# Kernel tuning notes

Measured on AMD Instinct MI355X. Metric: run time of the kernel, lower is better.

The kernel has to match this reference:

```python
import jax, jax.numpy as jnp
import numpy as np

B, N, D, H = 2048, 512, 128, 256
TRADE_K, N_BEST, CONF_TH = 10, 50, 0.05


def setup_inputs() -> dict:
    key = jax.random.key(0)
    ks = jax.random.split(key, 5)
    return {
        "signal_features": jax.random.normal(ks[0], (B, N, D), jnp.float32),
        "spread": jax.random.uniform(ks[1], (B, N), jnp.float32, minval=1e-4, maxval=0.01),
        "volatility": jax.random.uniform(ks[2], (B, N), jnp.float32, minval=1e-4, maxval=0.05),
        "W1": jax.random.normal(ks[3], (D, H), jnp.float32) / np.sqrt(D).astype(np.float32),
        "b1": jnp.zeros((H,), jnp.float32),
        "W2": jax.random.normal(ks[4], (H, 1), jnp.float32) / np.sqrt(H).astype(np.float32),
        "b2": jnp.zeros((1,), jnp.float32),
    }


def _scatter_mask(idx, n):
    # idx: [B, k] int32 -> bool mask [B, n] with True at idx positions
    b = idx.shape[0]
    return jnp.zeros((b, n), bool).at[jnp.arange(b)[:, None], idx].set(True)


def reference(signal_features, spread, volatility, W1, b1, W2, b2):
    # signal predictor: per-asset MLP with sigmoid head -> [B, N]
    h = jax.nn.relu(jnp.einsum('bnd,dh->bnh', signal_features, W1) + b1)
    signal_repr = jax.nn.sigmoid(jnp.einsum('bnh,ho->bno', h, W2)[..., 0] + b2[0])
    ls_score = signal_repr - 0.5  # allow_short_positions=True

    n_best = min(N_BEST, N)
    valid_spread = jnp.isfinite(spread) & (spread > 0)
    ratio = jnp.where(valid_spread, volatility / (spread + 1e-8), -jnp.inf)
    _, best_idx = jax.lax.top_k(ratio, n_best)
    universe_mask = _scatter_mask(best_idx, N)
    # rows with no valid spread: whole universe allowed
    universe_mask = universe_mask | ~valid_spread.any(axis=1, keepdims=True)

    masked_abs = jnp.where(universe_mask, jnp.abs(ls_score), -jnp.inf)
    k = min(TRADE_K, n_best)
    _, top_idx = jax.lax.top_k(masked_abs, k)
    mask = _scatter_mask(top_idx, N)

    selected = jnp.where(mask, ls_score, 0.0)
    action = selected / (jnp.sum(jnp.abs(selected), axis=1, keepdims=True) + 1e-8)

    confidence = masked_abs.max(axis=1)
    confidence = jnp.where(jnp.isfinite(confidence), confidence, 0.0)
    take_trade = (confidence >= CONF_TH).astype(action.dtype)[:, None]
    action = action * take_trade
    return action, confidence
```

## Files before the change

kernel.cpp:

```cpp
#include <hip/hip_runtime.h>
#include <hip/hip_bf16.h>
#include <math.h>

#define B_ 2048
#define N_ 512
#define D_ 128
#define H_ 256
#define BANDf 2e-4f

typedef __attribute__((ext_vector_type(8))) short bf16x8;
typedef __attribute__((ext_vector_type(4))) float f32x4;

__device__ __forceinline__ short f2bf(float x) {
    unsigned u = __float_as_uint(x);
    u = u + 0x7fffu + ((u >> 16) & 1u);
    return (short)(u >> 16);
}
__device__ __forceinline__ float bf2f(short h) {
    return __uint_as_float(((unsigned)(unsigned short)h) << 16);
}
__device__ __forceinline__ unsigned cvt_pk_bf16(float a, float b) {
    unsigned r;
    asm("v_cvt_pk_bf16_f32 %0, %1, %2" : "=v"(r) : "v"(a), "v"(b));
    return r;
}
template<int K>
__device__ __forceinline__ float dpp_shr_add(float zz) {
    int s = __builtin_amdgcn_update_dpp(0, __float_as_int(zz), 0x110 | K, 0xf, 0xf, true);
    return zz + __int_as_float(s);
}

__global__ __launch_bounds__(256) void pack_w(const float* __restrict__ W1,
                                              short* __restrict__ WpH,
                                              short* __restrict__ WpL)
{
    int tid = blockIdx.x * 256 + threadIdx.x;
    int l  = tid & 63;
    int ks = (tid >> 6) & 3;
    int nf = tid >> 8;
    int n  = nf * 16 + (l & 15);
    int kb = ks * 32 + ((l >> 4) << 3);
    bf16x8 hi, lo;
    #pragma unroll
    for (int j = 0; j < 8; ++j) {
        float w = W1[(size_t)(kb + j) * H_ + n];
        short h = f2bf(w);
        hi[j] = h;
        lo[j] = f2bf(w - bf2f(h));
    }
    *(bf16x8*)&WpH[(size_t)tid * 8] = hi;
    *(bf16x8*)&WpL[(size_t)tid * 8] = lo;
}

__global__ __launch_bounds__(256, 2) void mlp_mfma(
    const float* __restrict__ X, const short* __restrict__ WpH,
    const short* __restrict__ WpL, const float* __restrict__ b1,
    const float* __restrict__ W2, const float* __restrict__ b2,
    float* __restrict__ ls)
{
    __shared__ short Xh[64 * 128];
    __shared__ short Xl[64 * 128];
    __shared__ float zl[256];

    const int t    = threadIdx.x;
    const int lane = t & 63;
    const int wn   = t >> 6;
    const size_t m0 = (size_t)blockIdx.x * 64;

    const bf16x8* WH = (const bf16x8*)WpH;
    const bf16x8* WL = (const bf16x8*)WpL;

    bf16x8 Bhi[4][4];
    #pragma unroll
    for (int q = 0; q < 4; ++q)
        #pragma unroll
        for (int ks = 0; ks < 4; ++ks)
            Bhi[q][ks] = WH[((wn * 4 + q) * 4 + ks) * 64 + lane];

    bf16x8 Blo[2][4];
    #pragma unroll
    for (int q = 0; q < 4; ++q)
        Blo[0][q] = WL[((wn * 4 + q) * 4 + 0) * 64 + lane];

    {
        const float4* Xg = (const float4*)(X + m0 * D_);
        #pragma unroll
        for (int i = 0; i < 8; ++i) {
            int f = t + i * 256;
            float4 v = Xg[f];
            int row = f >> 5, k0 = (f & 31) << 2;
            unsigned h01 = cvt_pk_bf16(v.x, v.y);
            unsigned h23 = cvt_pk_bf16(v.z, v.w);
            float l0 = v.x - __uint_as_float(h01 << 16);
            float l1 = v.y - __uint_as_float(h01 & 0xffff0000u);
            float l2 = v.z - __uint_as_float(h23 << 16);
            float l3 = v.w - __uint_as_float(h23 & 0xffff0000u);
            unsigned lo01 = cvt_pk_bf16(l0, l1);
            unsigned lo23 = cvt_pk_bf16(l2, l3);
            int sidx = (row * 128 + k0) ^ ((row & 7) << 3);
            *(uint2*)&Xh[sidx] = make_uint2(h01, h23);
            *(uint2*)&Xl[sidx] = make_uint2(lo01, lo23);
        }
    }
    __syncthreads();

    f32x4 acc[4][4];
    #pragma unroll
    for (int mf = 0; mf < 4; ++mf)
        #pragma unroll
        for (int q = 0; q < 4; ++q)
            acc[mf][q] = (f32x4){0.f, 0.f, 0.f, 0.f};

    __builtin_amdgcn_s_setprio(1);
    #pragma unroll
    for (int ks = 0; ks < 4; ++ks) {
        const int cur = ks & 1, nxt = cur ^ 1;
        if (ks < 3) {
            #pragma unroll
            for (int q = 0; q < 4; ++q)
                Blo[nxt][q] = WL[((wn * 4 + q) * 4 + ks + 1) * 64 + lane];
        }
        #pragma unroll
        for (int mf = 0; mf < 4; ++mf) {
            int r = mf * 16 + (lane & 15);
            int sidx = (r * 128 + ks * 32 + ((lane >> 4) << 3)) ^ ((r & 7) << 3);
            bf16x8 Ah = *(const bf16x8*)&Xh[sidx];
            bf16x8 Al = *(const bf16x8*)&Xl[sidx];
            #pragma unroll
            for (int q = 0; q < 4; ++q) {
                acc[mf][q] = __builtin_amdgcn_mfma_f32_16x16x32_bf16(Ah, Bhi[q][ks],  acc[mf][q], 0, 0, 0);
                acc[mf][q] = __builtin_amdgcn_mfma_f32_16x16x32_bf16(Al, Bhi[q][ks],  acc[mf][q], 0, 0, 0);
                acc[mf][q] = __builtin_amdgcn_mfma_f32_16x16x32_bf16(Ah, Blo[cur][q], acc[mf][q], 0, 0, 0);
            }
        }
    }
    __builtin_amdgcn_s_setprio(0);

    float b1v[4], w2v[4];
    #pragma unroll
    for (int q = 0; q < 4; ++q) {
        int c = wn * 64 + q * 16 + (lane & 15);
        b1v[q] = b1[c];
        w2v[q] = W2[c];
    }
    #pragma unroll
    for (int mf = 0; mf < 4; ++mf) {
        #pragma unroll
        for (int i = 0; i < 4; ++i) {
            float zz = 0.f;
            #pragma unroll
            for (int q = 0; q < 4; ++q) {
                float h = acc[mf][q][i] + b1v[q];
                h = h > 0.f ? h : 0.f;
                zz += h * w2v[q];
            }
            zz = dpp_shr_add<1>(zz);
            zz = dpp_shr_add<2>(zz);
            zz = dpp_shr_add<4>(zz);
            zz = dpp_shr_add<8>(zz);
            if ((lane & 15) == 15) zl[wn * 64 + mf * 16 + ((lane >> 4) << 2) + i] = zz;
        }
    }
    __syncthreads();
    if (t < 64) {
        float z = zl[t] + zl[64 + t] + zl[128 + t] + zl[192 + t] + b2[0];
        ls[m0 + t] = 1.f / (1.f + expf(-z)) - 0.5f;
    }
}

__device__ __forceinline__ unsigned f2key(float f) {
    unsigned u = __float_as_uint(f);
    return (u & 0x80000000u) ? ~u : (u | 0x80000000u);
}
__device__ __forceinline__ float key2f(unsigned k) {
    return __uint_as_float((k & 0x80000000u) ? (k & 0x7fffffffu) : ~k);
}
__device__ __forceinline__ int lane_lt_count(unsigned long long m) {
    return __builtin_amdgcn_mbcnt_hi((unsigned)(m >> 32),
           __builtin_amdgcn_mbcnt_lo((unsigned)m, 0));
}

__device__ __forceinline__ void radix_topk(const unsigned (&key)[8], int k,
                                           unsigned &T, int &need)
{
    unsigned prefix = 0, maskhi = 0;
    int kk = k;
    for (int bit = 31; bit >= 0; --bit) {
        unsigned b = 1u << bit;
        int cnt1 = 0;
        #pragma unroll
        for (int j = 0; j < 8; ++j) {
            bool one = ((key[j] & maskhi) == prefix) && (key[j] & b);
            cnt1 += __popcll(__ballot(one));
        }
        if (cnt1 >= kk) prefix |= b; else kk -= cnt1;
        maskhi |= b;
    }
    T = prefix; need = kk;
}

__device__ __forceinline__ void tie_member(const unsigned (&key)[8], unsigned T,
                                           int need, bool (&mem)[8])
{
    int base = 0;
    #pragma unroll
    for (int j = 0; j < 8; ++j) {
        unsigned long long eb = __ballot(key[j] == T);
        int r = base + lane_lt_count(eb);
        mem[j] = (key[j] > T) || ((key[j] == T) && (r < need));
        base += __popcll(eb);
    }
}

__global__ __launch_bounds__(256) void select_kernel(
    const float* __restrict__ ls, const float* __restrict__ spread,
    const float* __restrict__ vol, const float* __restrict__ X,
    const float* __restrict__ W1, const float* __restrict__ b1,
    const float* __restrict__ W2, const float* __restrict__ b2,
    float* __restrict__ action, float* __restrict__ conf_out)
{
    const int t = threadIdx.x;
    const int l = t & 63;
    const int w = t >> 6;
    const int b = blockIdx.x * 4 + w;
    const size_t base = (size_t)b * N_;

    float rv[8], lsv[8];
    unsigned kr[8];
    bool anyv = false;
    #pragma unroll
    for (int j = 0; j < 8; ++j) {
        int n = l + (j << 6);
        float sp = spread[base + n];
        float vo = vol[base + n];
        bool valid = isfinite(sp) && (sp > 0.f);
        rv[j]  = valid ? (vo / (sp + 1e-8f)) : -INFINITY;
        lsv[j] = ls[base + n];
        anyv |= valid;
        kr[j] = f2key(rv[j]);
    }
    bool allow_all = (__any((int)anyv) == 0);

    unsigned T50; int need50;
    radix_topk(kr, 50, T50, need50);
    bool mem50[8];
    tie_member(kr, T50, need50, mem50);

    float mabs[8];
    unsigned km[8];
    #pragma unroll
    for (int j = 0; j < 8; ++j) {
        bool u = allow_all || mem50[j];
        mabs[j] = u ? fabsf(lsv[j]) : -INFINITY;
        km[j] = f2key(mabs[j]);
    }
    unsigned T10; int need10;
    radix_topk(km, 10, T10, need10);
    bool mem10[8];
    tie_member(km, T10, need10, mem10);
    float b10 = key2f(T10);

    float zp = 0.f, cf = -INFINITY;
    #pragma unroll
    for (int j = 0; j < 8; ++j) {
        if (mem10[j]) zp += mabs[j];
        cf = fmaxf(cf, mabs[j]);
    }
    #pragma unroll
    for (int s = 1; s < 64; s <<= 1) {
        zp += __shfl_xor(zp, s, 64);
        cf = fmaxf(cf, __shfl_xor(cf, s, 64));
    }
    float conf = cf;

    bool confclose = fabsf(conf - 0.05f) <= BANDf;
    bool inband[8];
    int nb = 0;
    #pragma unroll
    for (int j = 0; j < 8; ++j) {
        inband[j] = (mabs[j] != -INFINITY) && (fabsf(mabs[j] - b10) <= BANDf);
        nb += __popcll(__ballot(inband[j]));
    }
    bool redo = (nb >= 2) || confclose;

    if (!redo) {
        float cfin  = isfinite(conf) ? conf : 0.f;
        float scale = (cfin >= 0.05f) ? (1.f / (zp + 1e-8f)) : 0.f;
        #pragma unroll
        for (int j = 0; j < 8; ++j) {
            int n = l + (j << 6);
            action[base + n] = mem10[j] ? lsv[j] * scale : 0.f;
        }
        if (l == 0) conf_out[b] = cfin;
        return;
    }

    const float2* xr2 = (const float2*)&X[base * D_];
    float4 bb = *(const float4*)&b1[l * 4];
    float4 ww = *(const float4*)&W2[l * 4];
    const float b2v = b2[0];

    #pragma unroll
    for (int j = 0; j < 8; ++j) {
        bool cand = (nb >= 2 && inband[j]) || (confclose && mabs[j] == conf);
        unsigned long long bal = __ballot(cand);
        while (bal) {
            int s = __ffsll((long long)bal) - 1;
            bal &= bal - 1;
            int asset = s + (j << 6);
            float2 x2 = xr2[(size_t)asset * 64 + l];
            float h0 = 0.f, h1 = 0.f, h2 = 0.f, h3 = 0.f;
            #pragma unroll 16
            for (int kk = 0; kk < D_; ++kk) {
                float xk = __shfl((kk & 1) ? x2.y : x2.x, kk >> 1, 64);
                float4 wv = *(const float4*)&W1[(size_t)kk * H_ + l * 4];
                h0 += xk * wv.x; h1 += xk * wv.y; h2 += xk * wv.z; h3 += xk * wv.w;
            }
            h0 += bb.x; h1 += bb.y; h2 += bb.z; h3 += bb.w;
            float zz = (h0 > 0.f ? h0 : 0.f) * ww.x + (h1 > 0.f ? h1 : 0.f) * ww.y
                     + (h2 > 0.f ? h2 : 0.f) * ww.z + (h3 > 0.f ? h3 : 0.f) * ww.w;
            #pragma unroll
            for (int sh = 1; sh < 64; sh <<= 1) zz += __shfl_xor(zz, sh, 64);
            float val = 1.f / (1.f + expf(-(zz + b2v))) - 0.5f;
            if (l == s) {
                lsv[j]  = val;
                mabs[j] = fabsf(val);
                km[j]   = f2key(mabs[j]);
            }
        }
    }

    unsigned T10b; int need10b;
    radix_topk(km, 10, T10b, need10b);
    bool mem10b[8];
    tie_member(km, T10b, need10b, mem10b);

    float zx = 0.f, cfx = -INFINITY;
    #pragma unroll
    for (int j = 0; j < 8; ++j) {
        if (mem10b[j]) zx += mabs[j];
        cfx = fmaxf(cfx, mabs[j]);
    }
    #pragma unroll
    for (int s = 1; s < 64; s <<= 1) {
        zx += __shfl_xor(zx, s, 64);
        cfx = fmaxf(cfx, __shfl_xor(cfx, s, 64));
    }
    cfx = isfinite(cfx) ? cfx : 0.f;
    float scale = (cfx >= 0.05f) ? (1.f / (zx + 1e-8f)) : 0.f;
    #pragma unroll
    for (int j = 0; j < 8; ++j) {
        int n = l + (j << 6);
        action[base + n] = mem10b[j] ? lsv[j] * scale : 0.f;
    }
    if (l == 0) conf_out[b] = cfx;
}

extern "C" void kernel_launch(void* const* d_in, const int* in_sizes, int n_in,
                              void* d_out, int out_size, void* d_ws, size_t ws_size,
                              hipStream_t stream)
{
    const float* X  = (const float*)d_in[0];
    const float* sp = (const float*)d_in[1];
    const float* vo = (const float*)d_in[2];
    const float* W1 = (const float*)d_in[3];
    const float* b1 = (const float*)d_in[4];
    const float* W2 = (const float*)d_in[5];
    const float* b2 = (const float*)d_in[6];

    float* action = (float*)d_out;
    float* conf   = action + (size_t)B_ * N_;

    float* ls = (float*)d_ws;
    size_t need = (size_t)B_ * N_ * 4 + 2 * (size_t)D_ * H_ * 2;
    short *WpH, *WpL;
    if (ws_size >= need) {
        WpH = (short*)((char*)d_ws + (size_t)B_ * N_ * 4);
        WpL = WpH + (size_t)D_ * H_;
    } else {
        WpH = (short*)(action + (size_t)out_size - 2 * (size_t)D_ * H_ / 2);
        WpL = WpH + (size_t)D_ * H_;
    }

    hipLaunchKernelGGL(pack_w, dim3(16), dim3(256), 0, stream, W1, WpH, WpL);
    hipLaunchKernelGGL(mlp_mfma, dim3((B_ * N_) / 64), dim3(256), 0, stream,
                       X, WpH, WpL, b1, W2, b2, ls);
    hipLaunchKernelGGL(select_kernel, dim3(B_ / 4), dim3(256), 0, stream,
                       ls, sp, vo, X, W1, b1, W2, b2, action, conf);
}
```

Before: 278.6 us.

## Double MLP row tile to 128 and stream W1 fragments per k-step

The MLP kernel now handles 128 rows per block instead of 64. This halves the block count and reuses each W1 fragment load across twice as many MFMA tiles. To make room for the doubled accumulators (8x4 f32x4), the hi W1 fragments are no longer all kept in registers up front. Both hi and lo fragments are now double-buffered per k-step from global/L2. The cost is twice the LDS per block (64KB for X hi/lo) and higher register pressure, which may cut occupancy below the requested 2 blocks/CU and reduce latency hiding.

```diff
diff --git a/kernel.cpp b/kernel.cpp
--- a/kernel.cpp
+++ b/kernel.cpp
@@ -7,6 +7,7 @@
 #define D_ 128
 #define H_ 256
 #define BANDf 2e-4f
+#define TILE_M 128
 
 typedef __attribute__((ext_vector_type(8))) short bf16x8;
 typedef __attribute__((ext_vector_type(4))) float f32x4;
@@ -58,34 +59,29 @@
     const float* __restrict__ W2, const float* __restrict__ b2,
     float* __restrict__ ls)
 {
-    __shared__ short Xh[64 * 128];
-    __shared__ short Xl[64 * 128];
-    __shared__ float zl[256];
+    __shared__ short Xh[TILE_M * 128];
+    __shared__ short Xl[TILE_M * 128];
+    __shared__ float zl[512];
 
     const int t    = threadIdx.x;
     const int lane = t & 63;
     const int wn   = t >> 6;
-    const size_t m0 = (size_t)blockIdx.x * 64;
+    const size_t m0 = (size_t)blockIdx.x * TILE_M;
 
     const bf16x8* WH = (const bf16x8*)WpH;
     const bf16x8* WL = (const bf16x8*)WpL;
 
-    bf16x8 Bhi[4][4];
-    #pragma unroll
-    for (int q = 0; q < 4; ++q)
-        #pragma unroll
-        for (int ks = 0; ks < 4; ++ks)
-            Bhi[q][ks] = WH[((wn * 4 + q) * 4 + ks) * 64 + lane];
-
-    bf16x8 Blo[2][4];
-    #pragma unroll
-    for (int q = 0; q < 4; ++q)
-        Blo[0][q] = WL[((wn * 4 + q) * 4 + 0) * 64 + lane];
+    bf16x8 Bh[2][4], Bl[2][4];
+    #pragma unroll
+    for (int q = 0; q < 4; ++q) {
+        Bh[0][q] = WH[((wn * 4 + q) * 4 + 0) * 64 + lane];
+        Bl[0][q] = WL[((wn * 4 + q) * 4 + 0) * 64 + lane];
+    }
 
     {
         const float4* Xg = (const float4*)(X + m0 * D_);
         #pragma unroll
-        for (int i = 0; i < 8; ++i) {
+        for (int i = 0; i < 16; ++i) {
             int f = t + i * 256;
             float4 v = Xg[f];
             int row = f >> 5, k0 = (f & 31) << 2;
@@ -104,9 +100,9 @@
     }
     __syncthreads();
 
-    f32x4 acc[4][4];
-    #pragma unroll
-    for (int mf = 0; mf < 4; ++mf)
+    f32x4 acc[8][4];
+    #pragma unroll
+    for (int mf = 0; mf < 8; ++mf)
         #pragma unroll
         for (int q = 0; q < 4; ++q)
             acc[mf][q] = (f32x4){0.f, 0.f, 0.f, 0.f};
@@ -117,20 +113,22 @@
         const int cur = ks & 1, nxt = cur ^ 1;
         if (ks < 3) {
             #pragma unroll
-            for (int q = 0; q < 4; ++q)
-                Blo[nxt][q] = WL[((wn * 4 + q) * 4 + ks + 1) * 64 + lane];
-        }
-        #pragma unroll
-        for (int mf = 0; mf < 4; ++mf) {
+            for (int q = 0; q < 4; ++q) {
+                Bh[nxt][q] = WH[((wn * 4 + q) * 4 + ks + 1) * 64 + lane];
+                Bl[nxt][q] = WL[((wn * 4 + q) * 4 + ks + 1) * 64 + lane];
+            }
+        }
+        #pragma unroll
+        for (int mf = 0; mf < 8; ++mf) {
             int r = mf * 16 + (lane & 15);
             int sidx = (r * 128 + ks * 32 + ((lane >> 4) << 3)) ^ ((r & 7) << 3);
             bf16x8 Ah = *(const bf16x8*)&Xh[sidx];
             bf16x8 Al = *(const bf16x8*)&Xl[sidx];
             #pragma unroll
             for (int q = 0; q < 4; ++q) {
-                acc[mf][q] = __builtin_amdgcn_mfma_f32_16x16x32_bf16(Ah, Bhi[q][ks],  acc[mf][q], 0, 0, 0);
-                acc[mf][q] = __builtin_amdgcn_mfma_f32_16x16x32_bf16(Al, Bhi[q][ks],  acc[mf][q], 0, 0, 0);
-                acc[mf][q] = __builtin_amdgcn_mfma_f32_16x16x32_bf16(Ah, Blo[cur][q], acc[mf][q], 0, 0, 0);
+                acc[mf][q] = __builtin_amdgcn_mfma_f32_16x16x32_bf16(Ah, Bh[cur][q], acc[mf][q], 0, 0, 0);
+                acc[mf][q] = __builtin_amdgcn_mfma_f32_16x16x32_bf16(Al, Bh[cur][q], acc[mf][q], 0, 0, 0);
+                acc[mf][q] = __builtin_amdgcn_mfma_f32_16x16x32_bf16(Ah, Bl[cur][q], acc[mf][q], 0, 0, 0);
             }
         }
     }
@@ -144,7 +142,7 @@
         w2v[q] = W2[c];
     }
     #pragma unroll
-    for (int mf = 0; mf < 4; ++mf) {
+    for (int mf = 0; mf < 8; ++mf) {
         #pragma unroll
         for (int i = 0; i < 4; ++i) {
             float zz = 0.f;
@@ -158,12 +156,12 @@
             zz = dpp_shr_add<2>(zz);
             zz = dpp_shr_add<4>(zz);
             zz = dpp_shr_add<8>(zz);
-            if ((lane & 15) == 15) zl[wn * 64 + mf * 16 + ((lane >> 4) << 2) + i] = zz;
+            if ((lane & 15) == 15) zl[wn * 128 + mf * 16 + ((lane >> 4) << 2) + i] = zz;
         }
     }
     __syncthreads();
-    if (t < 64) {
-        float z = zl[t] + zl[64 + t] + zl[128 + t] + zl[192 + t] + b2[0];
+    if (t < TILE_M) {
+        float z = zl[t] + zl[128 + t] + zl[256 + t] + zl[384 + t] + b2[0];
         ls[m0 + t] = 1.f / (1.f + expf(-z)) - 0.5f;
     }
 }
@@ -383,7 +381,7 @@
     }
 
     hipLaunchKernelGGL(pack_w, dim3(16), dim3(256), 0, stream, W1, WpH, WpL);
-    hipLaunchKernelGGL(mlp_mfma, dim3((B_ * N_) / 64), dim3(256), 0, stream,
+    hipLaunchKernelGGL(mlp_mfma, dim3((B_ * N_) / TILE_M), dim3(256), 0, stream,
                        X, WpH, WpL, b1, W2, b2, ls);
     hipLaunchKernelGGL(select_kernel, dim3(B_ / 4), dim3(256), 0, stream,
                        ls, sp, vo, X, W1, b1, W2, b2, action, conf);
```

New measurement: 285.2 us. +2.4%, slower.

## Warp-specialize MLP kernel with producer waves double-buffering X tiles across 8 tiles

Applied to the files above, without the earlier changes.

Makes the MLP kernel persistent-ish: each 512-thread block processes 8 consecutive 64-row tiles. Four producer waves load and split X into bf16 hi/lo in a double-buffered LDS, while four consumer waves keep the W1 fragments in registers and run the MFMAs. The goal is to overlap the global X loads with compute and to amortize the W1 register loads across tiles. The costs are a doubled LDS footprint and a whole-block barrier per tile. Only half the waves issue MFMAs, and there are far fewer blocks to hide latency.

```diff
diff --git a/kernel.cpp b/kernel.cpp
--- a/kernel.cpp
+++ b/kernel.cpp
@@ -7,6 +7,7 @@
 #define D_ 128
 #define H_ 256
 #define BANDf 2e-4f
+#define NT_ 8
 
 typedef __attribute__((ext_vector_type(8))) short bf16x8;
 typedef __attribute__((ext_vector_type(4))) float f32x4;
@@ -52,41 +53,30 @@
     *(bf16x8*)&WpL[(size_t)tid * 8] = lo;
 }
 
-__global__ __launch_bounds__(256, 2) void mlp_mfma(
+__global__ __launch_bounds__(512, 2) void mlp_mfma(
     const float* __restrict__ X, const short* __restrict__ WpH,
     const short* __restrict__ WpL, const float* __restrict__ b1,
     const float* __restrict__ W2, const float* __restrict__ b2,
     float* __restrict__ ls)
 {
-    __shared__ short Xh[64 * 128];
-    __shared__ short Xl[64 * 128];
-    __shared__ float zl[256];
+    __shared__ short Xh[2][64 * 128];
+    __shared__ short Xl[2][64 * 128];
+    __shared__ float zl[2][256];
 
     const int t    = threadIdx.x;
     const int lane = t & 63;
     const int wn   = t >> 6;
-    const size_t m0 = (size_t)blockIdx.x * 64;
+    const int base_tile = blockIdx.x * NT_;
 
     const bf16x8* WH = (const bf16x8*)WpH;
     const bf16x8* WL = (const bf16x8*)WpL;
 
-    bf16x8 Bhi[4][4];
-    #pragma unroll
-    for (int q = 0; q < 4; ++q)
-        #pragma unroll
-        for (int ks = 0; ks < 4; ++ks)
-            Bhi[q][ks] = WH[((wn * 4 + q) * 4 + ks) * 64 + lane];
-
-    bf16x8 Blo[2][4];
-    #pragma unroll
-    for (int q = 0; q < 4; ++q)
-        Blo[0][q] = WL[((wn * 4 + q) * 4 + 0) * 64 + lane];
-
-    {
-        const float4* Xg = (const float4*)(X + m0 * D_);
+    auto stage = [&](int tl, int nb) {
+        const float4* Xg = (const float4*)(X + (size_t)tl * 64 * D_);
+        const int pt = t & 255;
         #pragma unroll
         for (int i = 0; i < 8; ++i) {
-            int f = t + i * 256;
+            int f = pt + i * 256;
             float4 v = Xg[f];
             int row = f >> 5, k0 = (f & 31) << 2;
             unsigned h01 = cvt_pk_bf16(v.x, v.y);
@@ -98,73 +88,104 @@
             unsigned lo01 = cvt_pk_bf16(l0, l1);
             unsigned lo23 = cvt_pk_bf16(l2, l3);
             int sidx = (row * 128 + k0) ^ ((row & 7) << 3);
-            *(uint2*)&Xh[sidx] = make_uint2(h01, h23);
-            *(uint2*)&Xl[sidx] = make_uint2(lo01, lo23);
-        }
+            *(uint2*)&Xh[nb][sidx] = make_uint2(h01, h23);
+            *(uint2*)&Xl[nb][sidx] = make_uint2(lo01, lo23);
+        }
+    };
+
+    bf16x8 Bhi[4][4], Blo[2][4];
+    float b1v[4], w2v[4], b2v = 0.f;
+
+    if (wn < 4) {
+        #pragma unroll
+        for (int q = 0; q < 4; ++q)
+            #pragma unroll
+            for (int ks = 0; ks < 4; ++ks)
+                Bhi[q][ks] = WH[((wn * 4 + q) * 4 + ks) * 64 + lane];
+        #pragma unroll
+        for (int q = 0; q < 4; ++q)
+            Blo[0][q] = WL[((wn * 4 + q) * 4 + 0) * 64 + lane];
+        #pragma unroll
+        for (int q = 0; q < 4; ++q) {
+            int c = wn * 64 + q * 16 + (lane & 15);
+            b1v[q] = b1[c];
+            w2v[q] = W2[c];
+        }
+        b2v = b2[0];
+    } else {
+        stage(base_tile, 0);
     }
     __syncthreads();
 
-    f32x4 acc[4][4];
-    #pragma unroll
-    for (int mf = 0; mf < 4; ++mf)
-        #pragma unroll
-        for (int q = 0; q < 4; ++q)
-            acc[mf][q] = (f32x4){0.f, 0.f, 0.f, 0.f};
-
-    __builtin_amdgcn_s_setprio(1);
-    #pragma unroll
-    for (int ks = 0; ks < 4; ++ks) {
-        const int cur = ks & 1, nxt = cur ^ 1;
-        if (ks < 3) {
+    for (int it = 0; it < NT_; ++it) {
+        const int cur = it & 1;
+
+        if (wn >= 4) {
+            if (it + 1 < NT_) stage(base_tile + it + 1, cur ^ 1);
+        } else {
+            if (it > 0 && t < 64) {
+                const int pb = cur ^ 1;
+                float z = zl[pb][t] + zl[pb][64 + t] + zl[pb][128 + t] + zl[pb][192 + t] + b2v;
+                ls[(size_t)(base_tile + it - 1) * 64 + t] = 1.f / (1.f + expf(-z)) - 0.5f;
+            }
+
+            f32x4 acc[4][4];
             #pragma unroll
-            for (int q = 0; q < 4; ++q)
-                Blo[nxt][q] = WL[((wn * 4 + q) * 4 + ks + 1) * 64 + lane];
-        }
-        #pragma unroll
-        for (int mf = 0; mf < 4; ++mf) {
-            int r = mf * 16 + (lane & 15);
-            int sidx = (r * 128 + ks * 32 + ((lane >> 4) << 3)) ^ ((r & 7) << 3);
-            bf16x8 Ah = *(const bf16x8*)&Xh[sidx];
-            bf16x8 Al = *(const bf16x8*)&Xl[sidx];
+            for (int mf = 0; mf < 4; ++mf)
+                #pragma unroll
+                for (int q = 0; q < 4; ++q)
+                    acc[mf][q] = (f32x4){0.f, 0.f, 0.f, 0.f};
+
+            __builtin_amdgcn_s_setprio(1);
             #pragma unroll
-            for (int q = 0; q < 4; ++q) {
-                acc[mf][q] = __builtin_amdgcn_mfma_f32_16x16x32_bf16(Ah, Bhi[q][ks],  acc[mf][q], 0, 0, 0);
-                acc[mf][q] = __builtin_amdgcn_mfma_f32_16x16x32_bf16(Al, Bhi[q][ks],  acc[mf][q], 0, 0, 0);
-                acc[mf][q] = __builtin_amdgcn_mfma_f32_16x16x32_bf16(Ah, Blo[cur][q], acc[mf][q], 0, 0, 0);
+            for (int ks = 0; ks < 4; ++ks) {
+                const int bc = ks & 1, bn = bc ^ 1;
+                const int nk = (ks + 1) & 3;
+                #pragma unroll
+                for (int q = 0; q < 4; ++q)
+                    Blo[bn][q] = WL[((wn * 4 + q) * 4 + nk) * 64 + lane];
+                #pragma unroll
+                for (int mf = 0; mf < 4; ++mf) {
+                    int r = mf * 16 + (lane & 15);
+                    int sidx = (r * 128 + ks * 32 + ((lane >> 4) << 3)) ^ ((r & 7) << 3);
+                    bf16x8 Ah = *(const bf16x8*)&Xh[cur][sidx];
+                    bf16x8 Al = *(const bf16x8*)&Xl[cur][sidx];
+                    #pragma unroll
+                    for (int q = 0; q < 4; ++q) {
+                        acc[mf][q] = __builtin_amdgcn_mfma_f32_16x16x32_bf16(Ah, Bhi[q][ks], acc[mf][q], 0, 0, 0);
+                        acc[mf][q] = __builtin_amdgcn_mfma_f32_16x16x32_bf16(Al, Bhi[q][ks], acc[mf][q], 0, 0, 0);
+                        acc[mf][q] = __builtin_amdgcn_mfma_f32_16x16x32_bf16(Ah, Blo[bc][q], acc[mf][q], 0, 0, 0);
+                    }
+                }
             }
-        }
-    }
-    __builtin_amdgcn_s_setprio(0);
-
-    float b1v[4], w2v[4];
-    #pragma unroll
-    for (int q = 0; q < 4; ++q) {
-        int c = wn * 64 + q * 16 + (lane & 15);
-        b1v[q] = b1[c];
-        w2v[q] = W2[c];
-    }
-    #pragma unroll
-    for (int mf = 0; mf < 4; ++mf) {
-        #pragma unroll
-        for (int i = 0; i < 4; ++i) {
-            float zz = 0.f;
+            __builtin_amdgcn_s_setprio(0);
+
             #pragma unroll
-            for (int q = 0; q < 4; ++q) {
-                float h = acc[mf][q][i] + b1v[q];
-                h = h > 0.f ? h : 0.f;
-                zz += h * w2v[q];
+            for (int mf = 0; mf < 4; ++mf) {
+                #pragma unroll
+                for (int i = 0; i < 4; ++i) {
+                    float zz = 0.f;
+                    #pragma unroll
+                    for (int q = 0; q < 4; ++q) {
+                        float h = acc[mf][q][i] + b1v[q];
+                        h = h > 0.f ? h : 0.f;
+                        zz += h * w2v[q];
+                    }
+                    zz = dpp_shr_add<1>(zz);
+                    zz = dpp_shr_add<2>(zz);
+                    zz = dpp_shr_add<4>(zz);
+                    zz = dpp_shr_add<8>(zz);
+                    if ((lane & 15) == 15) zl[cur][wn * 64 + mf * 16 + ((lane >> 4) << 2) + i] = zz;
+                }
             }
-            zz = dpp_shr_add<1>(zz);
-            zz = dpp_shr_add<2>(zz);
-            zz = dpp_shr_add<4>(zz);
-            zz = dpp_shr_add<8>(zz);
-            if ((lane & 15) == 15) zl[wn * 64 + mf * 16 + ((lane >> 4) << 2) + i] = zz;
-        }
-    }
-    __syncthreads();
+        }
+        __syncthreads();
+    }
+
     if (t < 64) {
-        float z = zl[t] + zl[64 + t] + zl[128 + t] + zl[192 + t] + b2[0];
-        ls[m0 + t] = 1.f / (1.f + expf(-z)) - 0.5f;
+        const int pb = (NT_ - 1) & 1;
+        float z = zl[pb][t] + zl[pb][64 + t] + zl[pb][128 + t] + zl[pb][192 + t] + b2v;
+        ls[(size_t)(base_tile + NT_ - 1) * 64 + t] = 1.f / (1.f + expf(-z)) - 0.5f;
     }
 }
 
@@ -383,7 +404,7 @@
     }
 
     hipLaunchKernelGGL(pack_w, dim3(16), dim3(256), 0, stream, W1, WpH, WpL);
-    hipLaunchKernelGGL(mlp_mfma, dim3((B_ * N_) / 64), dim3(256), 0, stream,
+    hipLaunchKernelGGL(mlp_mfma, dim3((B_ * N_) / (64 * NT_)), dim3(512), 0, stream,
                        X, WpH, WpL, b1, W2, b2, ls);
     hipLaunchKernelGGL(select_kernel, dim3(B_ / 4), dim3(256), 0, stream,
                        ls, sp, vo, X, W1, b1, W2, b2, action, conf);
```

Result: slower. 348.2 us (+25.0%).
